# Performance work log

Measured on AMD Instinct MI355X. Metric: run time of the kernel, lower is better.

Reference implementation:

```python
import jax, jax.numpy as jnp
import numpy as np
from jax import lax

B, C_IN, C_OUT, K, N_W, L = 32, 256, 256, 7, 8, 4096
SQ = C_IN // 32  # squeezed dim = 8
STRIDE, PAD = 1, 3


def setup_inputs() -> dict:
    key = jax.random.key(0)
    ks = jax.random.split(key, 8)
    s = 0.05
    return {
        "x": jax.random.normal(ks[0], (B, C_IN, L), dtype=jnp.float32),
        "conv_weight": jax.random.normal(ks[1], (C_OUT, C_IN, K, N_W), dtype=jnp.float32) * s,
        "w1": jax.random.normal(ks[2], (C_IN, SQ), dtype=jnp.float32) * s,   # linear1 weight (x @ w1)
        "b1": jax.random.normal(ks[3], (SQ,), dtype=jnp.float32) * s,
        "wk": jax.random.normal(ks[4], (SQ, K), dtype=jnp.float32) * s,      # kernel head
        "wi": jax.random.normal(ks[5], (SQ, C_IN), dtype=jnp.float32) * s,   # inc head
        "wo": jax.random.normal(ks[6], (SQ, C_OUT), dtype=jnp.float32) * s,  # outc head
        "wn": jax.random.normal(ks[7], (SQ, N_W), dtype=jnp.float32) * s,    # nums head
    }


def reference(x, conv_weight, w1, b1, wk, wi, wo, wn):
    # SqueezeFeedForward: AdaptiveAvgPool1d(1) == mean over length, then Linear + exact GELU
    pooled = jnp.mean(x, axis=-1)                        # [B, C_in]
    h = jax.nn.gelu(pooled @ w1 + b1, approximate=False)  # [B, SQ]

    kr = jax.nn.sigmoid(h @ wk)          # [B, K]
    inc = jax.nn.sigmoid(h @ wi)         # [B, C_in]
    outc = jax.nn.sigmoid(h @ wo)        # [B, C_out]
    nums = jax.nn.softmax(h @ wn, -1)    # [B, N_w]

    # Per-sample mixed weights: sum over num_weight of 4-way outer-product gated base weight
    w = jnp.einsum('bk,bi,bo,bn,oikn->boik', kr, inc, outc, nums, conv_weight)  # [B,O,I,K]

    b, o, i, k = w.shape
    l = x.shape[-1]
    # Batched per-sample conv via grouped conv: groups = B
    lhs = x.reshape(1, b * i, l)         # [1, B*I, L]
    rhs = w.reshape(b * o, i, k)         # [B*O, I, K]
    out = lax.conv_general_dilated(
        lhs, rhs,
        window_strides=(STRIDE,),
        padding=[(PAD, PAD)],
        dimension_numbers=('NCH', 'OIH', 'NCH'),
        feature_group_count=b,
    )
    return out.reshape(b, o, -1)         # [B, O, L_out]
```

## Files before the change

kernel.cpp:

```cpp
#include <hip/hip_runtime.h>
#include <hip/hip_bf16.h>
#include <math.h>

#define B_   32
#define CI   256
#define CO   256
#define KW   7
#define NW   8
#define SQD  8
#define L_   4096
#define PITCH 272

typedef __attribute__((ext_vector_type(8)))  __bf16 bf16x8;
typedef __attribute__((ext_vector_type(4)))  __bf16 bf16x4;
typedef __attribute__((ext_vector_type(4)))  float  f32x4;
typedef __attribute__((ext_vector_type(16))) float  f32x16;

static __device__ __forceinline__ unsigned short f2bf(float f) {
    unsigned int u = __builtin_bit_cast(unsigned int, f);
    u += 0x7FFFu + ((u >> 16) & 1u);
    return (unsigned short)(u >> 16);
}
static __device__ __forceinline__ uint2 pack4bf(float a, float b, float c, float d) {
    bf16x4 v;
    v[0] = (__bf16)a; v[1] = (__bf16)b; v[2] = (__bf16)c; v[3] = (__bf16)d;
    return __builtin_bit_cast(uint2, v);
}

__global__ __launch_bounds__(256) void k1_mean(
        const float* __restrict__ x, float* __restrict__ pooled) {
    int row = blockIdx.x;
    const float* p = x + (size_t)row * L_;
    int t = threadIdx.x;
    float s = 0.f;
#pragma unroll
    for (int it = 0; it < 4; ++it) {
        float4 v = *(const float4*)(p + (size_t)(t + 256 * it) * 4);
        s += v.x + v.y + v.z + v.w;
    }
    for (int m = 1; m <= 32; m <<= 1) s += __shfl_xor(s, m);
    __shared__ float wsum[4];
    if ((t & 63) == 0) wsum[t >> 6] = s;
    __syncthreads();
    if (t == 0)
        pooled[row] = (wsum[0] + wsum[1] + wsum[2] + wsum[3]) * (1.0f / L_);
}

__global__ __launch_bounds__(64) void k2_gates(
        const float* __restrict__ pooled,
        const float* __restrict__ w1, const float* __restrict__ b1,
        const float* __restrict__ wk, const float* __restrict__ wi,
        const float* __restrict__ wo, const float* __restrict__ wn,
        float* __restrict__ kr, float* __restrict__ inc,
        float* __restrict__ outc, float* __restrict__ nums)
{
    int b = blockIdx.x, lane = threadIdx.x;
    float pc[4];
#pragma unroll
    for (int j = 0; j < 4; ++j)
        pc[j] = pooled[b * CI + lane + 64 * j];
    float h[SQD];
#pragma unroll
    for (int s = 0; s < SQD; ++s) {
        float ps = 0.f;
#pragma unroll
        for (int j = 0; j < 4; ++j)
            ps += pc[j] * w1[(lane + 64 * j) * SQD + s];
        for (int m = 1; m <= 32; m <<= 1) ps += __shfl_xor(ps, m);
        float z = ps + b1[s];
        h[s] = 0.5f * z * (1.0f + erff(z * 0.70710678118654752f));
    }
    if (lane < KW) {
        float a = 0.f;
#pragma unroll
        for (int s = 0; s < SQD; ++s) a += h[s] * wk[s * KW + lane];
        kr[b * 8 + lane] = 1.0f / (1.0f + expf(-a));
    }
    if (lane < NW) {
        float e[NW]; float mx = -1e30f;
#pragma unroll
        for (int n = 0; n < NW; ++n) {
            float a = 0.f;
#pragma unroll
            for (int s = 0; s < SQD; ++s) a += h[s] * wn[s * NW + n];
            e[n] = a; mx = fmaxf(mx, a);
        }
        float den = 0.f;
#pragma unroll
        for (int n = 0; n < NW; ++n) den += expf(e[n] - mx);
        nums[b * NW + lane] = expf(e[lane] - mx) / den;
    }
#pragma unroll
    for (int j = 0; j < 4; ++j) {
        int c = lane + 64 * j;
        float a = 0.f, o2 = 0.f;
#pragma unroll
        for (int s = 0; s < SQD; ++s) {
            a  += h[s] * wi[s * CI + c];
            o2 += h[s] * wo[s * CO + c];
        }
        inc[b * CI + c]  = 1.0f / (1.0f + expf(-a));
        outc[b * CO + c] = 1.0f / (1.0f + expf(-o2));
    }
}

__global__ __launch_bounds__(256) void k3_wgen(
        const float* __restrict__ cw,
        const float* __restrict__ kr, const float* __restrict__ inc,
        const float* __restrict__ outc, const float* __restrict__ nums,
        unsigned short* __restrict__ W2) {
    __shared__ float s_nums[B_][NW];
    __shared__ float s_kr[B_][KW];
    __shared__ float s_inc[B_][32];
    __shared__ float s_outc[B_][8];
    int t = threadIdx.x;
    int ic = blockIdx.x & 7, o0 = (blockIdx.x >> 3) * 8;
    s_nums[t >> 3][t & 7] = nums[t];
    if (t < B_ * KW) s_kr[t / KW][t % KW] = kr[(t / KW) * 8 + (t % KW)];
    for (int u = t; u < 32 * 32; u += 256) {
        int bb = u >> 5, ii = u & 31;
        s_inc[bb][ii] = inc[bb * CI + ic * 32 + ii];
    }
    for (int u = t; u < 32 * 8; u += 256) {
        int bb = u >> 3, oo = u & 7;
        s_outc[bb][oo] = outc[bb * CO + o0 + oo];
    }
    __syncthreads();
    int ii = t & 31, oo = t >> 5;
    int o = o0 + oo, i = ic * 32 + ii;
    float cwv[KW][NW];
    const float* p = cw + ((size_t)(o * CI + i)) * (KW * NW);
#pragma unroll
    for (int k = 0; k < KW; ++k)
#pragma unroll
        for (int n = 0; n < NW; ++n) cwv[k][n] = p[k * NW + n];
    for (int bb = 0; bb < B_; ++bb) {
        float gio = s_inc[bb][ii] * s_outc[bb][oo];
#pragma unroll
        for (int k = 0; k < KW; ++k) {
            float sk = 0.f;
#pragma unroll
            for (int n = 0; n < NW; ++n) sk += s_nums[bb][n] * cwv[k][n];
            float w = s_kr[bb][k] * gio * sk;
            W2[(((size_t)(bb * KW + k) * 8 + ic) * CO + o) * 32 + ii] = f2bf(w);
        }
    }
}

__global__ __launch_bounds__(256, 2) void k4_conv(
        const float* __restrict__ x,
        const unsigned short* __restrict__ W2,
        float* __restrict__ out) {
    __shared__ __align__(16) unsigned short xs[134 * PITCH];
    int bid = blockIdx.x;
    int wg  = (bid & 7) * 128 + (bid >> 3);
    int b = wg >> 5, l0 = (wg & 31) * 128;
    int t = threadIdx.x;
    const float* xb = x + (size_t)b * CI * L_;

    {
        int u = t >> 3;
        int lam = t & 7;
        int i0 = u * 8;
#pragma unroll
        for (int it = 0; it < 4; ++it) {
            int ch = lam + 8 * it;
            const float* src = xb + (size_t)i0 * L_ + l0 + ch * 4;
            float4 f[8];
#pragma unroll
            for (int e = 0; e < 8; ++e)
                f[e] = *(const float4*)(src + (size_t)e * L_);
#pragma unroll
            for (int j = 0; j < 4; ++j) {
                int r = ch * 4 + j + 3;
                uint2 a = pack4bf((&f[0].x)[j], (&f[1].x)[j], (&f[2].x)[j], (&f[3].x)[j]);
                uint2 c = pack4bf((&f[4].x)[j], (&f[5].x)[j], (&f[6].x)[j], (&f[7].x)[j]);
                uint4 w; w.x = a.x; w.y = a.y; w.z = c.x; w.w = c.y;
                *(uint4*)(xs + r * PITCH + u * 8) = w;
            }
        }
    }
    if (t < 192) {
        int h = t >> 5, u = t & 31;
        int r = (h < 3) ? h : (128 + h);
        int gl = l0 - 3 + r;
        bool ok = (gl >= 0 && gl < L_);
        float f[8];
#pragma unroll
        for (int e = 0; e < 8; ++e)
            f[e] = ok ? xb[(size_t)(u * 8 + e) * L_ + gl] : 0.f;
        uint2 a = pack4bf(f[0], f[1], f[2], f[3]);
        uint2 c = pack4bf(f[4], f[5], f[6], f[7]);
        uint4 w; w.x = a.x; w.y = a.y; w.z = c.x; w.w = c.y;
        *(uint4*)(xs + r * PITCH + u * 8) = w;
    }
    __syncthreads();

    int lane = t & 63, wid = t >> 6;
    int o_base = wid * 64;
    int ml = lane & 31, khalf = lane >> 5;

    f32x16 acc[2][4];
#pragma unroll
    for (int a = 0; a < 2; ++a)
#pragma unroll
        for (int c = 0; c < 4; ++c)
#pragma unroll
            for (int q = 0; q < 16; ++q) acc[a][c][q] = 0.f;

    const unsigned short* wA = W2 + (size_t)b * (56 * CO * 32)
                               + (o_base + ml) * 32 + khalf * 8;
    const unsigned short* xB = xs + (size_t)ml * PITCH + khalf * 8;

    auto LOADF = [&](bf16x8 (&AF)[2], bf16x8 (&BF)[4], int S) {
        int k_ = S >> 4, icc_ = (S >> 1) & 7, half_ = S & 1;
        size_t aoff = (size_t)(k_ * 8 + icc_) * (CO * 32) + half_ * 16;
#pragma unroll
        for (int mt = 0; mt < 2; ++mt)
            AF[mt] = *(const bf16x8*)(wA + aoff + mt * 32 * 32);
        int boff = k_ * PITCH + icc_ * 32 + half_ * 16;
#pragma unroll
        for (int nt = 0; nt < 4; ++nt)
            BF[nt] = *(const bf16x8*)(xB + boff + nt * 32 * PITCH);
    };
    auto DOMFMA = [&](bf16x8 (&AF)[2], bf16x8 (&BF)[4]) {
        __builtin_amdgcn_s_setprio(1);
#pragma unroll
        for (int mt = 0; mt < 2; ++mt)
#pragma unroll
            for (int nt = 0; nt < 4; ++nt)
                acc[mt][nt] = __builtin_amdgcn_mfma_f32_32x32x16_bf16(
                    AF[mt], BF[nt], acc[mt][nt], 0, 0, 0);
        __builtin_amdgcn_s_setprio(0);
    };

    int base = wid * 28;
    bf16x8 afA[2], bfA[4], afB[2], bfB[4];
    LOADF(afA, bfA, base);
    for (int ss = 0; ss < 112; ss += 2) {
        int S1 = ss + 1 + base; if (S1 >= 112) S1 -= 112;
        LOADF(afB, bfB, S1);
        DOMFMA(afA, bfA);
        if (ss + 2 < 112) {
            int S2 = ss + 2 + base; if (S2 >= 112) S2 -= 112;
            LOADF(afA, bfA, S2);
        }
        DOMFMA(afB, bfB);
    }

#pragma unroll
    for (int mt = 0; mt < 2; ++mt)
#pragma unroll
        for (int nt = 0; nt < 4; ++nt) {
            int l = l0 + nt * 32 + ml;
#pragma unroll
            for (int q = 0; q < 16; ++q) {
                int o = o_base + mt * 32 + (q & 3) + 8 * (q >> 2) + 4 * khalf;
                out[((size_t)(b * CO + o)) * L_ + l] = acc[mt][nt][q];
            }
        }
}

extern "C" void kernel_launch(void* const* d_in, const int* in_sizes, int n_in,
                              void* d_out, int out_size, void* d_ws, size_t ws_size,
                              hipStream_t stream) {
    const float* x  = (const float*)d_in[0];
    const float* cw = (const float*)d_in[1];
    const float* w1 = (const float*)d_in[2];
    const float* b1 = (const float*)d_in[3];
    const float* wk = (const float*)d_in[4];
    const float* wi = (const float*)d_in[5];
    const float* wo = (const float*)d_in[6];
    const float* wn = (const float*)d_in[7];
    float* out = (float*)d_out;

    char* ws = (char*)d_ws;
    unsigned short* W2 = (unsigned short*)(ws + 0);
    float* pooled = (float*)(ws + 29360128);
    float* kr     = (float*)(ws + 29392896);
    float* inc    = (float*)(ws + 29393920);
    float* outc   = (float*)(ws + 29426688);
    float* nums   = (float*)(ws + 29459456);

    k1_mean<<<B_ * CI, 256, 0, stream>>>(x, pooled);
    k2_gates<<<B_, 64, 0, stream>>>(pooled, w1, b1, wk, wi, wo, wn,
                                    kr, inc, outc, nums);
    k3_wgen<<<256, 256, 0, stream>>>(cw, kr, inc, outc, nums, W2);
    k4_conv<<<1024, 256, 0, stream>>>(x, W2, out);
}
```

Baseline: 194.5 us.

## Retile conv MFMA waves into 128x64 output tiles and shrink LDS pitch

Changes the per-wave work split from 64 output channels by 128 positions to 128 output channels by 64 positions, arranged as a 2x2 grid of waves. Each pipeline step now loads both K-halves of a (k, channel-chunk) pair at once. The rotated per-wave start offset is removed, so all waves walk the reduction in the same order. The LDS row pitch drops from 272 to 264 to change the bank-conflict pattern. The intent is to alter the balance between global weight loads and LDS activation loads, and to improve LDS access. It doubles the fragment registers per stage, and waves now hit the same weight addresses at the same time.

```diff
diff --git a/kernel.cpp b/kernel.cpp
--- a/kernel.cpp
+++ b/kernel.cpp
@@ -9,11 +9,10 @@
 #define NW   8
 #define SQD  8
 #define L_   4096
-#define PITCH 272
+#define PITCH 264
 
 typedef __attribute__((ext_vector_type(8)))  __bf16 bf16x8;
 typedef __attribute__((ext_vector_type(4)))  __bf16 bf16x4;
-typedef __attribute__((ext_vector_type(4)))  float  f32x4;
 typedef __attribute__((ext_vector_type(16))) float  f32x16;
 
 static __device__ __forceinline__ unsigned short f2bf(float f) {
@@ -197,62 +196,63 @@
     __syncthreads();
 
     int lane = t & 63, wid = t >> 6;
-    int o_base = wid * 64;
+    int o_base = (wid & 1) * 128;
+    int l_wave = (wid >> 1) * 64;
     int ml = lane & 31, khalf = lane >> 5;
 
-    f32x16 acc[2][4];
-#pragma unroll
-    for (int a = 0; a < 2; ++a)
-#pragma unroll
-        for (int c = 0; c < 4; ++c)
+    f32x16 acc[4][2];
+#pragma unroll
+    for (int a = 0; a < 4; ++a)
+#pragma unroll
+        for (int c = 0; c < 2; ++c)
 #pragma unroll
             for (int q = 0; q < 16; ++q) acc[a][c][q] = 0.f;
 
     const unsigned short* wA = W2 + (size_t)b * (56 * CO * 32)
                                + (o_base + ml) * 32 + khalf * 8;
-    const unsigned short* xB = xs + (size_t)ml * PITCH + khalf * 8;
-
-    auto LOADF = [&](bf16x8 (&AF)[2], bf16x8 (&BF)[4], int S) {
-        int k_ = S >> 4, icc_ = (S >> 1) & 7, half_ = S & 1;
-        size_t aoff = (size_t)(k_ * 8 + icc_) * (CO * 32) + half_ * 16;
-#pragma unroll
-        for (int mt = 0; mt < 2; ++mt)
-            AF[mt] = *(const bf16x8*)(wA + aoff + mt * 32 * 32);
-        int boff = k_ * PITCH + icc_ * 32 + half_ * 16;
-#pragma unroll
-        for (int nt = 0; nt < 4; ++nt)
-            BF[nt] = *(const bf16x8*)(xB + boff + nt * 32 * PITCH);
+    const unsigned short* xB = xs + (size_t)(l_wave + ml) * PITCH + khalf * 8;
+
+    auto LOADP = [&](bf16x8 (&AF)[2][4], bf16x8 (&BF)[2][2], int P) {
+        int k_ = P >> 3, icc_ = P & 7;
+        const unsigned short* ap = wA + (size_t)P * (CO * 32);
+        int boff = k_ * PITCH + icc_ * 32;
+#pragma unroll
+        for (int h = 0; h < 2; ++h) {
+#pragma unroll
+            for (int mt = 0; mt < 4; ++mt)
+                AF[h][mt] = *(const bf16x8*)(ap + h * 16 + mt * 32 * 32);
+#pragma unroll
+            for (int nt = 0; nt < 2; ++nt)
+                BF[h][nt] = *(const bf16x8*)(xB + boff + h * 16 + nt * 32 * PITCH);
+        }
     };
-    auto DOMFMA = [&](bf16x8 (&AF)[2], bf16x8 (&BF)[4]) {
+    auto DOP = [&](bf16x8 (&AF)[2][4], bf16x8 (&BF)[2][2]) {
         __builtin_amdgcn_s_setprio(1);
 #pragma unroll
-        for (int mt = 0; mt < 2; ++mt)
-#pragma unroll
-            for (int nt = 0; nt < 4; ++nt)
-                acc[mt][nt] = __builtin_amdgcn_mfma_f32_32x32x16_bf16(
-                    AF[mt], BF[nt], acc[mt][nt], 0, 0, 0);
+        for (int h = 0; h < 2; ++h)
+#pragma unroll
+            for (int mt = 0; mt < 4; ++mt)
+#pragma unroll
+                for (int nt = 0; nt < 2; ++nt)
+                    acc[mt][nt] = __builtin_amdgcn_mfma_f32_32x32x16_bf16(
+                        AF[h][mt], BF[h][nt], acc[mt][nt], 0, 0, 0);
         __builtin_amdgcn_s_setprio(0);
     };
 
-    int base = wid * 28;
-    bf16x8 afA[2], bfA[4], afB[2], bfB[4];
-    LOADF(afA, bfA, base);
-    for (int ss = 0; ss < 112; ss += 2) {
-        int S1 = ss + 1 + base; if (S1 >= 112) S1 -= 112;
-        LOADF(afB, bfB, S1);
-        DOMFMA(afA, bfA);
-        if (ss + 2 < 112) {
-            int S2 = ss + 2 + base; if (S2 >= 112) S2 -= 112;
-            LOADF(afA, bfA, S2);
-        }
-        DOMFMA(afB, bfB);
-    }
-
-#pragma unroll
-    for (int mt = 0; mt < 2; ++mt)
-#pragma unroll
-        for (int nt = 0; nt < 4; ++nt) {
-            int l = l0 + nt * 32 + ml;
+    bf16x8 afA[2][4], bfA[2][2], afB[2][4], bfB[2][2];
+    LOADP(afA, bfA, 0);
+    for (int P = 0; P < 56; P += 2) {
+        LOADP(afB, bfB, P + 1);
+        DOP(afA, bfA);
+        if (P + 2 < 56) LOADP(afA, bfA, P + 2);
+        DOP(afB, bfB);
+    }
+
+#pragma unroll
+    for (int mt = 0; mt < 4; ++mt)
+#pragma unroll
+        for (int nt = 0; nt < 2; ++nt) {
+            int l = l0 + l_wave + nt * 32 + ml;
 #pragma unroll
             for (int q = 0; q < 16; ++q) {
                 int o = o_base + mt * 32 + (q & 3) + 8 * (q >> 2) + 4 * khalf;
```

After: 196.5 us. No clear change (+1.0%).
